# Optimization experiments

Hardware: AMD Instinct MI355X
Metric: run time of the kernel (lower is better)

Reference implementation:

```python
import jax, jax.numpy as jnp
import numpy as np

NUM_EXPERTS = 8
TOP_K = 2
CAPACITY_FACTOR = 1.25


def setup_inputs() -> dict:
    key = jax.random.key(0)
    ks = jax.random.split(key, 5)
    B, S, D, H, E = 4, 2048, 1024, 2048, NUM_EXPERTS
    scale = 0.02
    return {
        "x": jax.random.normal(ks[0], (B, S, D), dtype=jnp.float32),
        "gate_w": jax.random.normal(ks[1], (E, D), dtype=jnp.float32) * scale,
        "gate_proj_w": jax.random.normal(ks[2], (E, H, D), dtype=jnp.float32) * scale,
        "up_proj_w": jax.random.normal(ks[3], (E, H, D), dtype=jnp.float32) * scale,
        "down_proj_w": jax.random.normal(ks[4], (E, D, H), dtype=jnp.float32) * scale,
    }


def reference(x, gate_w, gate_proj_w, up_proj_w, down_proj_w):
    B, S, D = x.shape
    E, K = NUM_EXPERTS, TOP_K
    T = B * S
    xf = x.reshape(T, D)

    # Router: softmax over expert logits, then top-k (eval mode: no aux loss)
    logits = xf @ gate_w.T                      # (T, E)
    probs = jax.nn.softmax(logits, axis=-1)
    top_p, top_i = jax.lax.top_k(probs, K)      # (T, K)
    w = top_p / (jnp.sum(top_p, axis=-1, keepdims=True) + 1e-9)  # (T, K)

    # Capacity drop: per (k, expert), keep only the first `capacity` tokens
    # in token order (matches torch loop which truncates nonzero indices).
    capacity = int(CAPACITY_FACTOR * T / E)
    oh = jax.nn.one_hot(top_i, E, dtype=jnp.int32)        # (T, K, E)
    rank = jnp.cumsum(oh, axis=0) - 1                     # rank within (k, e)
    my_rank = jnp.sum(rank * oh, axis=-1)                 # (T, K)
    keep = (my_rank < capacity).astype(w.dtype)

    # Combined per-token per-expert weight (dropped tokens get 0)
    comb = jnp.einsum("tk,tke->te", w * keep, oh.astype(w.dtype))  # (T, E)

    # Per-expert dense SwiGLU; zero-weight tokens contribute nothing,
    # which matches the masked gather/scatter-add of the original.
    out = jnp.zeros_like(xf)
    for e in range(E):
        g = jax.nn.silu(xf @ gate_proj_w[e].T)   # (T, H)
        u = xf @ up_proj_w[e].T                  # (T, H)
        y = (g * u) @ down_proj_w[e].T           # (T, D)
        out = out + comb[:, e:e + 1] * y
    return out.reshape(B, S, D)
```

## Files before the change

### kernel.cpp

```cpp
#include <hip/hip_runtime.h>
#include <hip/hip_bf16.h>
#include <stdint.h>

#define T_TOK 8192
#define D_DIM 1024
#define H_DIM 2048
#define E_NUM 8
#define CAP   1280
#define CAP2  2560
#define MT_K  10

#define BM 128
#define BN 128
#define BN_GU 64
#define BK 32

typedef __attribute__((ext_vector_type(8))) short short8;
typedef __attribute__((ext_vector_type(4))) float float4v;
typedef __attribute__((address_space(1))) const unsigned int gu32;
typedef __attribute__((address_space(3))) unsigned int lu32;

static __device__ __forceinline__ unsigned short f2bf(float f) {
    unsigned int u = __float_as_uint(f);
    unsigned int r = (u + 0x7FFFu + ((u >> 16) & 1u)) >> 16;
    return (unsigned short)r;
}

static __device__ __forceinline__ void store4bf(unsigned short* d, float4 v) {
    union { unsigned short u[4]; uint2 q; } pk;
    pk.u[0] = f2bf(v.x); pk.u[1] = f2bf(v.y);
    pk.u[2] = f2bf(v.z); pk.u[3] = f2bf(v.w);
    *(uint2*)d = pk.q;
}

__global__ __launch_bounds__(256) void convert_w_k(
    const float* __restrict__ wg, const float* __restrict__ wu,
    const float* __restrict__ wd,
    unsigned short* __restrict__ wgbf, unsigned short* __restrict__ wubf,
    unsigned short* __restrict__ wdbf) {
    const int W4 = E_NUM * H_DIM * D_DIM / 4;
    const int total = 3 * W4;
    const int stride = gridDim.x * 256;
    for (int i = blockIdx.x * 256 + threadIdx.x; i < total; i += stride) {
        const float* s; unsigned short* d; int j;
        if (i < W4)          { s = wg; d = wgbf; j = i; }
        else if (i < 2 * W4) { s = wu; d = wubf; j = i - W4; }
        else                 { s = wd; d = wdbf; j = i - 2 * W4; }
        store4bf(d + (size_t)j * 4, ((const float4*)s)[j]);
    }
}

__global__ __launch_bounds__(256) void router_k(
    const float* __restrict__ x, const float* __restrict__ gw,
    int* __restrict__ topi, float* __restrict__ topw,
    unsigned short* __restrict__ xbf) {
    const int t = blockIdx.x * 4 + (threadIdx.x >> 6);
    const int lane = threadIdx.x & 63;
    const float* xr = x + (size_t)t * D_DIM;
    unsigned short* xbr = xbf + (size_t)t * D_DIM;

    float p[E_NUM];
#pragma unroll
    for (int e = 0; e < E_NUM; ++e) p[e] = 0.f;
#pragma unroll
    for (int c = 0; c < 4; ++c) {
        const int idx = c * 256 + lane * 4;
        const float4 xv = *(const float4*)(xr + idx);
        store4bf(xbr + idx, xv);
#pragma unroll
        for (int e = 0; e < E_NUM; ++e) {
            const float4 gv = *(const float4*)(gw + e * D_DIM + idx);
            p[e] += xv.x * gv.x + xv.y * gv.y + xv.z * gv.z + xv.w * gv.w;
        }
    }
#pragma unroll
    for (int e = 0; e < E_NUM; ++e) {
        float v = p[e];
#pragma unroll
        for (int off = 32; off >= 1; off >>= 1) v += __shfl_xor(v, off);
        p[e] = v;
    }
    if (lane == 0) {
        float mx = p[0];
#pragma unroll
        for (int e = 1; e < E_NUM; ++e) mx = fmaxf(mx, p[e]);
        float pe[E_NUM]; float s = 0.f;
#pragma unroll
        for (int e = 0; e < E_NUM; ++e) { pe[e] = expf(p[e] - mx); s += pe[e]; }
        const float inv = 1.f / s;
        int i0 = 0;
#pragma unroll
        for (int e = 1; e < E_NUM; ++e) if (pe[e] > pe[i0]) i0 = e;
        int i1 = -1;
#pragma unroll
        for (int e = 0; e < E_NUM; ++e) {
            if (e == i0) continue;
            if (i1 < 0 || pe[e] > pe[i1]) i1 = e;
        }
        const float p0 = pe[i0] * inv, p1 = pe[i1] * inv;
        const float wn = 1.f / (p0 + p1 + 1e-9f);
        topi[t * 2 + 0] = i0; topi[t * 2 + 1] = i1;
        topw[t * 2 + 0] = p0 * wn; topw[t * 2 + 1] = p1 * wn;
    }
}

__global__ __launch_bounds__(1024) void assign_k(
    const int* __restrict__ topi, const float* __restrict__ topw,
    int* __restrict__ tok_list, float* __restrict__ w_list,
    int* __restrict__ cnt) {
    __shared__ unsigned char topiL[T_TOK * 2];
    __shared__ int kept[2][E_NUM];
    const int tid = threadIdx.x;
    const int wid = tid >> 6, lane = tid & 63;
    const int k = wid >> 3, e = wid & 7;
    const uint64_t lt = (1ull << lane) - 1ull;

    for (int i = tid; i < T_TOK * 2 / 4; i += 1024) {
        const int4 v = ((const int4*)topi)[i];
        uchar4 b;
        b.x = (unsigned char)v.x; b.y = (unsigned char)v.y;
        b.z = (unsigned char)v.z; b.w = (unsigned char)v.w;
        ((uchar4*)topiL)[i] = b;
    }
    __syncthreads();

    int total = 0;
    for (int base = 0; base < T_TOK; base += 64) {
        const int idx = topiL[(base + lane) * 2 + k];
        total += __popcll(__ballot(idx == e));
    }
    if (lane == 0) {
        const int kc = min(total, CAP);
        kept[k][e] = kc;
        cnt[e * 2 + k] = kc;
    }
    __syncthreads();
    const int myBase = e * CAP2 + k * CAP;

    int running = 0, keptRun = 0;
    for (int base = 0; base < T_TOK; base += 64) {
        const int t = base + lane;
        const bool pred = (topiL[t * 2 + k] == e);
        const uint64_t m = __ballot(pred);
        const int rank = running + __popcll(m & lt);
        const bool keep = pred && (rank < CAP);
        const uint64_t km = __ballot(keep);
        if (keep) {
            const int slot = myBase + keptRun + __popcll(km & lt);
            tok_list[slot] = t;
            w_list[slot] = topw[t * 2 + k];
        }
        running += __popcll(m);
        keptRun += __popcll(km);
    }
    __syncthreads();
    for (int s = tid; s < E_NUM * CAP2; s += 1024) {
        const int ee = s / CAP2;
        const int rem = s - ee * CAP2;
        const int kk = rem / CAP, ls = rem - kk * CAP;
        if (ls >= kept[kk][ee]) { tok_list[s] = 0; w_list[s] = 0.f; }
    }
}

__global__ __launch_bounds__(256, 4) void gateup_bf_k(
    const unsigned short* __restrict__ xbf,
    const unsigned short* __restrict__ wgbf, const unsigned short* __restrict__ wubf,
    const int* __restrict__ tok_list, const int* __restrict__ cnt,
    unsigned short* __restrict__ h_ws, int e0) {
    const int ez = blockIdx.z;
    const int e = e0 + ez;
    const int kk = blockIdx.y / MT_K;
    const int m0 = (blockIdx.y - kk * MT_K) * BM;
    if (m0 >= cnt[e * 2 + kk]) return;
    const int n0 = blockIdx.x * BN_GU;
    const int sbase = e * CAP2 + kk * CAP + m0;
    const size_t hbase = (size_t)ez * CAP2 + kk * CAP + m0;

    __shared__ __align__(1024) unsigned short smem[16384];

    const int tid = threadIdx.x, wid = tid >> 6, lane = tid & 63;

    const unsigned short* gsrc[8];
    int ldsoff[8];
#pragma unroll
    for (int i = 0; i < 8; ++i) {
        const int f = (wid * 8 + i) * 64 + lane;
        const unsigned short* g;
        if (f < 1024) {
            const int r = f >> 3, c = (f & 7) ^ (r & 7);
            const int tok = tok_list[sbase + r];
            g = xbf + (size_t)tok * D_DIM + c * 8;
        } else if (f < 1536) {
            const int fr = f - 1024;
            const int r = fr >> 3, c = (fr & 7) ^ (r & 7);
            g = wgbf + ((size_t)e * H_DIM + n0 + r) * D_DIM + c * 8;
        } else {
            const int fr = f - 1536;
            const int r = fr >> 3, c = (fr & 7) ^ (r & 7);
            g = wubf + ((size_t)e * H_DIM + n0 + r) * D_DIM + c * 8;
        }
        gsrc[i] = g;
        ldsoff[i] = (wid * 8 + i) * 1024;
    }

    float4v accg[4][2], accu[4][2];
#pragma unroll
    for (int i = 0; i < 4; ++i)
#pragma unroll
        for (int j = 0; j < 2; ++j) {
            accg[i][j] = (float4v){0.f, 0.f, 0.f, 0.f};
            accu[i][j] = (float4v){0.f, 0.f, 0.f, 0.f};
        }

    const int wm = (wid & 1) * 64;
    const int wn = (wid >> 1) * 32;
    const int frow = lane & 15;
    const int quad = lane >> 4;

    for (int k0 = 0; k0 < D_DIM; k0 += 64) {
#pragma unroll
        for (int i = 0; i < 8; ++i)
            __builtin_amdgcn_global_load_lds(
                (gu32*)(gsrc[i] + k0),
                (lu32*)((char*)smem + ldsoff[i]), 16, 0, 0);
        __syncthreads();

#pragma unroll
        for (int s = 0; s < 2; ++s) {
            const int c = s * 4 + quad;
            short8 af[4], bgf[2], buf[2];
#pragma unroll
            for (int i = 0; i < 4; ++i) {
                const int row = wm + i * 16 + frow;
                af[i] = *(const short8*)&smem[(row * 8 + (c ^ (row & 7))) * 8];
            }
#pragma unroll
            for (int j = 0; j < 2; ++j) {
                const int row = wn + j * 16 + frow;
                bgf[j] = *(const short8*)&smem[8192 + (row * 8 + (c ^ (row & 7))) * 8];
                buf[j] = *(const short8*)&smem[12288 + (row * 8 + (c ^ (row & 7))) * 8];
            }
#pragma unroll
            for (int i = 0; i < 4; ++i)
#pragma unroll
                for (int j = 0; j < 2; ++j) {
                    accg[i][j] = __builtin_amdgcn_mfma_f32_16x16x32_bf16(af[i], bgf[j], accg[i][j], 0, 0, 0);
                    accu[i][j] = __builtin_amdgcn_mfma_f32_16x16x32_bf16(af[i], buf[j], accu[i][j], 0, 0, 0);
                }
        }
        __syncthreads();
    }

    const int col = lane & 15, rbase = (lane >> 4) * 4;
#pragma unroll
    for (int i = 0; i < 4; ++i)
#pragma unroll
        for (int j = 0; j < 2; ++j)
#pragma unroll
            for (int r = 0; r < 4; ++r) {
                const float g = accg[i][j][r];
                const float u = accu[i][j][r];
                const float hv = (g / (1.f + __expf(-g))) * u;
                const int m = wm + i * 16 + rbase + r;
                const int n = wn + j * 16 + col;
                h_ws[(hbase + m) * H_DIM + (n0 + n)] = f2bf(hv);
            }
}

__global__ __launch_bounds__(256, 3) void down_bf_k(
    const unsigned short* __restrict__ h_ws, const unsigned short* __restrict__ wdbf,
    const int* __restrict__ tok_list, const float* __restrict__ w_list,
    const int* __restrict__ cnt, float* __restrict__ out, int e0, int kk) {
    const int ez = blockIdx.z;
    const int e = e0 + ez;
    const int m0 = blockIdx.y * BM;
    const int nkept = cnt[e * 2 + kk];
    if (m0 >= nkept) return;
    const int n0 = blockIdx.x * BN;
    const int sbase = e * CAP2 + kk * CAP + m0;
    const size_t hbase = (size_t)ez * CAP2 + kk * CAP + m0;

    __shared__ __align__(1024) unsigned short smem[16384];
    __shared__ int tokL[BM];
    __shared__ float wL[BM];

    const int tid = threadIdx.x, wid = tid >> 6, lane = tid & 63;
    if (tid < BM) {
        tokL[tid] = tok_list[sbase + tid];
        wL[tid] = w_list[sbase + tid];
    }

    const unsigned short* gsrc[8];
    int ldsoff[8];
#pragma unroll
    for (int i = 0; i < 8; ++i) {
        const int f = (wid * 8 + i) * 64 + lane;
        const unsigned short* g;
        if (f < 1024) {
            const int r = f >> 3, c = (f & 7) ^ (r & 7);
            g = h_ws + (hbase + r) * H_DIM + c * 8;
        } else {
            const int fr = f - 1024;
            const int r = fr >> 3, c = (fr & 7) ^ (r & 7);
            g = wdbf + ((size_t)e * D_DIM + n0 + r) * H_DIM + c * 8;
        }
        gsrc[i] = g;
        ldsoff[i] = (wid * 8 + i) * 1024;
    }

    float4v acc[4][4];
#pragma unroll
    for (int i = 0; i < 4; ++i)
#pragma unroll
        for (int j = 0; j < 4; ++j) acc[i][j] = (float4v){0.f, 0.f, 0.f, 0.f};

    const int wm = (wid & 1) * 64, wn = (wid >> 1) * 64;
    const int frow = lane & 15;
    const int quad = lane >> 4;

    for (int k0 = 0; k0 < H_DIM; k0 += 64) {
#pragma unroll
        for (int i = 0; i < 8; ++i)
            __builtin_amdgcn_global_load_lds(
                (gu32*)(gsrc[i] + k0),
                (lu32*)((char*)smem + ldsoff[i]), 16, 0, 0);
        __syncthreads();

#pragma unroll
        for (int s = 0; s < 2; ++s) {
            const int c = s * 4 + quad;
            short8 af[4], bf[4];
#pragma unroll
            for (int i = 0; i < 4; ++i) {
                const int row = wm + i * 16 + frow;
                af[i] = *(const short8*)&smem[(row * 8 + (c ^ (row & 7))) * 8];
            }
#pragma unroll
            for (int j = 0; j < 4; ++j) {
                const int row = wn + j * 16 + frow;
                bf[j] = *(const short8*)&smem[8192 + (row * 8 + (c ^ (row & 7))) * 8];
            }
#pragma unroll
            for (int i = 0; i < 4; ++i)
#pragma unroll
                for (int j = 0; j < 4; ++j)
                    acc[i][j] = __builtin_amdgcn_mfma_f32_16x16x32_bf16(af[i], bf[j], acc[i][j], 0, 0, 0);
        }
        __syncthreads();
    }

    const int col = lane & 15, rbase = (lane >> 4) * 4;
#pragma unroll
    for (int i = 0; i < 4; ++i)
#pragma unroll
        for (int r = 0; r < 4; ++r) {
            const int m = wm + i * 16 + rbase + r;
            if (m0 + m >= nkept) continue;
            const float wRow = wL[m];
            float* orow = out + (size_t)tokL[m] * D_DIM + n0;
#pragma unroll
            for (int j = 0; j < 4; ++j) {
                const int n = j * 16 + wn + col;
                const float v = acc[i][j][r] * wRow;
                if (kk == 0) orow[n] = v;
                else         orow[n] += v;
            }
        }
}

__global__ __launch_bounds__(256, 2) void gateup_legacy_k(
    const float* __restrict__ x,
    const float* __restrict__ wg_all, const float* __restrict__ wu_all,
    const int* __restrict__ tok_list, const int* __restrict__ cnt,
    unsigned short* __restrict__ h_ws, int e0) {
    const int ez = blockIdx.z;
    const int e = e0 + ez;
    const int kk = blockIdx.y / MT_K;
    const int m0 = (blockIdx.y - kk * MT_K) * BM;
    if (m0 >= cnt[e * 2 + kk]) return;
    const int n0 = blockIdx.x * BN;
    const int sbase = e * CAP2 + kk * CAP + m0;
    const size_t hbase = (size_t)ez * CAP2 + kk * CAP + m0;

    __shared__ __align__(16) unsigned short As[BM][BK];
    __shared__ __align__(16) unsigned short Bg[BN][BK];
    __shared__ __align__(16) unsigned short Bu[BN][BK];
    __shared__ int tokL[BM];

    const int tid = threadIdx.x;
    if (tid < BM) tokL[tid] = tok_list[sbase + tid];
    __syncthreads();

    const float* wg = wg_all + (size_t)e * H_DIM * D_DIM;
    const float* wu = wu_all + (size_t)e * H_DIM * D_DIM;

    const float* aSrc[4]; const float* gSrc[4]; const float* uSrc[4];
    unsigned short* aDst[4]; unsigned short* gDst[4]; unsigned short* uDst[4];
#pragma unroll
    for (int it = 0; it < 4; ++it) {
        const int fid = it * 256 + tid;
        const int row = fid >> 3;
        const int c4 = (fid & 7) * 4;
        aSrc[it] = x + (size_t)tokL[row] * D_DIM + c4;
        gSrc[it] = wg + (size_t)(n0 + row) * D_DIM + c4;
        uSrc[it] = wu + (size_t)(n0 + row) * D_DIM + c4;
        aDst[it] = &As[row][c4];
        gDst[it] = &Bg[row][c4];
        uDst[it] = &Bu[row][c4];
    }

    float4v accg[4][4], accu[4][4];
#pragma unroll
    for (int i = 0; i < 4; ++i)
#pragma unroll
        for (int j = 0; j < 4; ++j) {
            accg[i][j] = (float4v){0.f, 0.f, 0.f, 0.f};
            accu[i][j] = (float4v){0.f, 0.f, 0.f, 0.f};
        }

    const int wid = tid >> 6, lane = tid & 63;
    const int wm = (wid & 1) * 64, wn = (wid >> 1) * 64;
    const int frow = lane & 15;
    const int fk = (lane >> 4) * 8;

    for (int k0 = 0; k0 < D_DIM; k0 += BK) {
#pragma unroll
        for (int it = 0; it < 4; ++it) {
            store4bf(aDst[it], *(const float4*)(aSrc[it] + k0));
            store4bf(gDst[it], *(const float4*)(gSrc[it] + k0));
            store4bf(uDst[it], *(const float4*)(uSrc[it] + k0));
        }
        __syncthreads();
        short8 af[4], bgf[4], buf[4];
#pragma unroll
        for (int i = 0; i < 4; ++i)
            af[i] = *(const short8*)&As[wm + i * 16 + frow][fk];
#pragma unroll
        for (int j = 0; j < 4; ++j) {
            bgf[j] = *(const short8*)&Bg[wn + j * 16 + frow][fk];
            buf[j] = *(const short8*)&Bu[wn + j * 16 + frow][fk];
        }
#pragma unroll
        for (int i = 0; i < 4; ++i)
#pragma unroll
            for (int j = 0; j < 4; ++j) {
                accg[i][j] = __builtin_amdgcn_mfma_f32_16x16x32_bf16(af[i], bgf[j], accg[i][j], 0, 0, 0);
                accu[i][j] = __builtin_amdgcn_mfma_f32_16x16x32_bf16(af[i], buf[j], accu[i][j], 0, 0, 0);
            }
        __syncthreads();
    }

    const int col = lane & 15, rbase = (lane >> 4) * 4;
#pragma unroll
    for (int i = 0; i < 4; ++i)
#pragma unroll
        for (int j = 0; j < 4; ++j)
#pragma unroll
            for (int r = 0; r < 4; ++r) {
                const float g = accg[i][j][r];
                const float u = accu[i][j][r];
                const float hv = (g / (1.f + __expf(-g))) * u;
                const int m = wm + i * 16 + rbase + r;
                const int n = wn + j * 16 + col;
                h_ws[(hbase + m) * H_DIM + (n0 + n)] = f2bf(hv);
            }
}

__global__ __launch_bounds__(256, 2) void down_legacy_k(
    const unsigned short* __restrict__ h_ws, const float* __restrict__ wd_all,
    const int* __restrict__ tok_list, const float* __restrict__ w_list,
    const int* __restrict__ cnt, float* __restrict__ out, int e0) {
    const int ez = blockIdx.z;
    const int e = e0 + ez;
    const int kk = blockIdx.y / MT_K;
    const int m0 = (blockIdx.y - kk * MT_K) * BM;
    if (m0 >= cnt[e * 2 + kk]) return;
    const int n0 = blockIdx.x * BN;
    const int sbase = e * CAP2 + kk * CAP + m0;
    const size_t hbase = (size_t)ez * CAP2 + kk * CAP + m0;

    __shared__ __align__(16) unsigned short As[BM][BK];
    __shared__ __align__(16) unsigned short Bs[BN][BK];
    __shared__ int tokL[BM];
    __shared__ float wL[BM];

    const int tid = threadIdx.x;
    if (tid < BM) {
        tokL[tid] = tok_list[sbase + tid];
        wL[tid] = w_list[sbase + tid];
    }
    __syncthreads();

    const unsigned short* hA = h_ws + hbase * H_DIM;
    const float* wd = wd_all + (size_t)e * D_DIM * H_DIM;

    const unsigned short* aSrc[2]; unsigned short* aDst[2];
#pragma unroll
    for (int it = 0; it < 2; ++it) {
        const int fid = it * 256 + tid;
        const int row = fid >> 2;
        const int c8 = (fid & 3) * 8;
        aSrc[it] = hA + (size_t)row * H_DIM + c8;
        aDst[it] = &As[row][c8];
    }
    const float* bSrc[4]; unsigned short* bDst[4];
#pragma unroll
    for (int it = 0; it < 4; ++it) {
        const int fid = it * 256 + tid;
        const int row = fid >> 3;
        const int c4 = (fid & 7) * 4;
        bSrc[it] = wd + (size_t)(n0 + row) * H_DIM + c4;
        bDst[it] = &Bs[row][c4];
    }

    float4v acc[4][4];
#pragma unroll
    for (int i = 0; i < 4; ++i)
#pragma unroll
        for (int j = 0; j < 4; ++j) acc[i][j] = (float4v){0.f, 0.f, 0.f, 0.f};

    const int wid = tid >> 6, lane = tid & 63;
    const int wm = (wid & 1) * 64, wn = (wid >> 1) * 64;
    const int frow = lane & 15;
    const int fk = (lane >> 4) * 8;

    for (int k0 = 0; k0 < H_DIM; k0 += BK) {
#pragma unroll
        for (int it = 0; it < 2; ++it)
            *(uint4*)aDst[it] = *(const uint4*)(aSrc[it] + k0);
#pragma unroll
        for (int it = 0; it < 4; ++it)
            store4bf(bDst[it], *(const float4*)(bSrc[it] + k0));
        __syncthreads();
        short8 af[4], bf[4];
#pragma unroll
        for (int i = 0; i < 4; ++i)
            af[i] = *(const short8*)&As[wm + i * 16 + frow][fk];
#pragma unroll
        for (int j = 0; j < 4; ++j)
            bf[j] = *(const short8*)&Bs[wn + j * 16 + frow][fk];
#pragma unroll
        for (int i = 0; i < 4; ++i)
#pragma unroll
            for (int j = 0; j < 4; ++j)
                acc[i][j] = __builtin_amdgcn_mfma_f32_16x16x32_bf16(af[i], bf[j], acc[i][j], 0, 0, 0);
        __syncthreads();
    }

    const int col = lane & 15, rbase = (lane >> 4) * 4;
#pragma unroll
    for (int i = 0; i < 4; ++i)
#pragma unroll
        for (int j = 0; j < 4; ++j)
#pragma unroll
            for (int r = 0; r < 4; ++r) {
                const int m = wm + i * 16 + rbase + r;
                const int n = wn + j * 16 + col;
                const float v = acc[i][j][r] * wL[m];
                unsafeAtomicAdd(&out[(size_t)tokL[m] * D_DIM + n0 + n], v);
            }
}

extern "C" void kernel_launch(void* const* d_in, const int* in_sizes, int n_in,
                              void* d_out, int out_size, void* d_ws, size_t ws_size,
                              hipStream_t stream) {
    const float* x        = (const float*)d_in[0];
    const float* gate_w   = (const float*)d_in[1];
    const float* gate_pw  = (const float*)d_in[2];
    const float* up_pw    = (const float*)d_in[3];
    const float* down_pw  = (const float*)d_in[4];
    float* out = (float*)d_out;
    (void)n_in; (void)in_sizes; (void)out_size;

    uint8_t* ws = (uint8_t*)d_ws;
    size_t off = 0;
    int*   topi     = (int*)(ws + off);   off += (size_t)T_TOK * 2 * 4;
    float* topw     = (float*)(ws + off); off += (size_t)T_TOK * 2 * 4;
    int*   tok_list = (int*)(ws + off);   off += (size_t)E_NUM * CAP2 * 4;
    float* w_list   = (float*)(ws + off); off += (size_t)E_NUM * CAP2 * 4;
    int*   cnt      = (int*)(ws + off);   off += 256;
    off = (off + 4095) & ~(size_t)4095;
    const size_t routing_end = off;

    const size_t x_elems = (size_t)T_TOK * D_DIM;
    const size_t w_elems = (size_t)E_NUM * H_DIM * D_DIM;
    unsigned short* xbf  = (unsigned short*)(ws + off); off += x_elems * 2;
    unsigned short* wgbf = (unsigned short*)(ws + off); off += w_elems * 2;
    unsigned short* wubf = (unsigned short*)(ws + off); off += w_elems * 2;
    unsigned short* wdbf = (unsigned short*)(ws + off); off += w_elems * 2;
    const size_t need_base = off;
    const size_t per_e = (size_t)CAP2 * H_DIM * 2;

    hipMemsetAsync(out, 0, (size_t)T_TOK * D_DIM * sizeof(float), stream);

    if (ws_size >= need_base + per_e) {
        unsigned short* h_ws = (unsigned short*)(ws + need_base);
        int chunk = (int)((ws_size - need_base) / per_e);
        if (chunk > E_NUM) chunk = E_NUM;

        router_k<<<T_TOK / 4, 256, 0, stream>>>(x, gate_w, topi, topw, xbf);
        assign_k<<<1, 1024, 0, stream>>>(topi, topw, tok_list, w_list, cnt);
        convert_w_k<<<4096, 256, 0, stream>>>(gate_pw, up_pw, down_pw,
                                              wgbf, wubf, wdbf);

        for (int e0 = 0; e0 < E_NUM; e0 += chunk) {
            const int ne = (e0 + chunk <= E_NUM) ? chunk : (E_NUM - e0);
            dim3 g1(H_DIM / BN_GU, 2 * MT_K, ne);
            gateup_bf_k<<<g1, 256, 0, stream>>>(xbf, wgbf, wubf, tok_list, cnt, h_ws, e0);
            dim3 g2(D_DIM / BN, MT_K, ne);
            down_bf_k<<<g2, 256, 0, stream>>>(h_ws, wdbf, tok_list, w_list, cnt, out, e0, 0);
            down_bf_k<<<g2, 256, 0, stream>>>(h_ws, wdbf, tok_list, w_list, cnt, out, e0, 1);
        }
    } else {
        unsigned short* h_ws = (unsigned short*)(ws + routing_end);
        int chunk = (ws_size > routing_end) ? (int)((ws_size - routing_end) / per_e) : 0;
        if (chunk > E_NUM) chunk = E_NUM;
        if (chunk < 1) chunk = 1;

        router_k<<<T_TOK / 4, 256, 0, stream>>>(x, gate_w, topi, topw, xbf);
        assign_k<<<1, 1024, 0, stream>>>(topi, topw, tok_list, w_list, cnt);

        for (int e0 = 0; e0 < E_NUM; e0 += chunk) {
            const int ne = (e0 + chunk <= E_NUM) ? chunk : (E_NUM - e0);
            dim3 g1(H_DIM / BN, 2 * MT_K, ne);
            gateup_legacy_k<<<g1, 256, 0, stream>>>(x, gate_pw, up_pw, tok_list, cnt, h_ws, e0);
            dim3 g2(D_DIM / BN, 2 * MT_K, ne);
            down_legacy_k<<<g2, 256, 0, stream>>>(h_ws, down_pw, tok_list, w_list, cnt, out, e0);
        }
    }
}
```

Before: 604.8 us.

## Fuse router with weight conversion and merge down-proj launches via atomics

Merges the router and the fp32-to-bf16 weight conversion into one prep kernel so routing blocks and conversion blocks run in the same grid. Stages the SwiGLU output tile through shared memory so h_ws gets 16-byte coalesced stores. Collapses the two per-k down-projection launches into one grid with k in blockIdx.z, using atomic adds into the pre-zeroed output, and raises the occupancy hint to 4. The atomics add contention and make the float summation order nondeterministic. The prep kernel also now writes its outputs into buffers that the routing-assignment kernel reads.

```diff
diff --git a/kernel.cpp b/kernel.cpp
--- a/kernel.cpp
+++ b/kernel.cpp
@@ -15,6 +15,9 @@
 #define BN_GU 64
 #define BK 32
 
+#define ROUTE_BLKS (T_TOK / 4)
+#define CONV_BLKS  4096
+
 typedef __attribute__((ext_vector_type(8))) short short8;
 typedef __attribute__((ext_vector_type(4))) float float4v;
 typedef __attribute__((address_space(1))) const unsigned int gu32;
@@ -33,20 +36,75 @@
     *(uint2*)d = pk.q;
 }
 
-__global__ __launch_bounds__(256) void convert_w_k(
+__global__ __launch_bounds__(256) void prep_k(
+    const float* __restrict__ x, const float* __restrict__ gw,
+    int* __restrict__ topi, float* __restrict__ topw,
+    unsigned short* __restrict__ xbf,
     const float* __restrict__ wg, const float* __restrict__ wu,
     const float* __restrict__ wd,
     unsigned short* __restrict__ wgbf, unsigned short* __restrict__ wubf,
     unsigned short* __restrict__ wdbf) {
-    const int W4 = E_NUM * H_DIM * D_DIM / 4;
-    const int total = 3 * W4;
-    const int stride = gridDim.x * 256;
-    for (int i = blockIdx.x * 256 + threadIdx.x; i < total; i += stride) {
-        const float* s; unsigned short* d; int j;
-        if (i < W4)          { s = wg; d = wgbf; j = i; }
-        else if (i < 2 * W4) { s = wu; d = wubf; j = i - W4; }
-        else                 { s = wd; d = wdbf; j = i - 2 * W4; }
-        store4bf(d + (size_t)j * 4, ((const float4*)s)[j]);
+    if (blockIdx.x < ROUTE_BLKS) {
+        const int t = blockIdx.x * 4 + (threadIdx.x >> 6);
+        const int lane = threadIdx.x & 63;
+        const float* xr = x + (size_t)t * D_DIM;
+        unsigned short* xbr = xbf + (size_t)t * D_DIM;
+
+        float p[E_NUM];
+#pragma unroll
+        for (int e = 0; e < E_NUM; ++e) p[e] = 0.f;
+#pragma unroll
+        for (int c = 0; c < 4; ++c) {
+            const int idx = c * 256 + lane * 4;
+            const float4 xv = *(const float4*)(xr + idx);
+            store4bf(xbr + idx, xv);
+#pragma unroll
+            for (int e = 0; e < E_NUM; ++e) {
+                const float4 gv = *(const float4*)(gw + e * D_DIM + idx);
+                p[e] += xv.x * gv.x + xv.y * gv.y + xv.z * gv.z + xv.w * gv.w;
+            }
+        }
+#pragma unroll
+        for (int e = 0; e < E_NUM; ++e) {
+            float v = p[e];
+#pragma unroll
+            for (int off = 32; off >= 1; off >>= 1) v += __shfl_xor(v, off);
+            p[e] = v;
+        }
+        if (lane == 0) {
+            float mx = p[0];
+#pragma unroll
+            for (int e = 1; e < E_NUM; ++e) mx = fmaxf(mx, p[e]);
+            float pe[E_NUM]; float s = 0.f;
+#pragma unroll
+            for (int e = 0; e < E_NUM; ++e) { pe[e] = expf(p[e] - mx); s += pe[e]; }
+            const float inv = 1.f / s;
+            int i0 = 0;
+#pragma unroll
+            for (int e = 1; e < E_NUM; ++e) if (pe[e] > pe[i0]) i0 = e;
+            int i1 = -1;
+#pragma unroll
+            for (int e = 0; e < E_NUM; ++e) {
+                if (e == i0) continue;
+                if (i1 < 0 || pe[e] > pe[i1]) i1 = e;
+            }
+            const float p0 = pe[i0] * inv, p1 = pe[i1] * inv;
+            const float wn = 1.f / (p0 + p1 + 1e-9f);
+            topi[t * 2 + 0] = i0; topi[t * 2 + 1] = i1;
+            topw[t * 2 + 0] = p0 * wn; topw[t * 2 + 1] = p1 * wn;
+        }
+    } else {
+        const int W4 = E_NUM * H_DIM * D_DIM / 4;
+        const int total = 3 * W4;
+        const int stride = CONV_BLKS * 256;
+        for (int i = (blockIdx.x - ROUTE_BLKS) * 256 + threadIdx.x; i < total;
+             i += stride) {
+            const float* s; unsigned short* d; int j;
+            if (i < W4)          { s = wg; d = wgbf; j = i; }
+            else if (i < 2 * W4) { s = wu; d = wubf; j = i - W4; }
+            else                 { s = wd; d = wdbf; j = i - 2 * W4; }
+            store4bf(d + (size_t)j * 4, ((const float4*)s)[j]);
+        }
     }
 }
 
@@ -263,15 +321,24 @@
                 const float hv = (g / (1.f + __expf(-g))) * u;
                 const int m = wm + i * 16 + rbase + r;
                 const int n = wn + j * 16 + col;
-                h_ws[(hbase + m) * H_DIM + (n0 + n)] = f2bf(hv);
-            }
-}
-
-__global__ __launch_bounds__(256, 3) void down_bf_k(
+                smem[m * 64 + n] = f2bf(hv);
+            }
+    __syncthreads();
+#pragma unroll
+    for (int c2 = 0; c2 < 4; ++c2) {
+        const int idx = c2 * 256 + tid;
+        const int row = idx >> 3, cc = (idx & 7) * 8;
+        *(uint4*)&h_ws[(hbase + row) * H_DIM + n0 + cc] =
+            *(const uint4*)&smem[row * 64 + cc];
+    }
+}
+
+__global__ __launch_bounds__(256, 4) void down_bf_k(
     const unsigned short* __restrict__ h_ws, const unsigned short* __restrict__ wdbf,
     const int* __restrict__ tok_list, const float* __restrict__ w_list,
-    const int* __restrict__ cnt, float* __restrict__ out, int e0, int kk) {
-    const int ez = blockIdx.z;
+    const int* __restrict__ cnt, float* __restrict__ out, int e0) {
+    const int ez = blockIdx.z >> 1;
+    const int kk = blockIdx.z & 1;
     const int e = e0 + ez;
     const int m0 = blockIdx.y * BM;
     const int nkept = cnt[e * 2 + kk];
@@ -361,9 +428,7 @@
 #pragma unroll
             for (int j = 0; j < 4; ++j) {
                 const int n = j * 16 + wn + col;
-                const float v = acc[i][j][r] * wRow;
-                if (kk == 0) orow[n] = v;
-                else         orow[n] += v;
+                unsafeAtomicAdd(&orow[n], acc[i][j][r] * wRow);
             }
         }
 }
@@ -598,18 +663,17 @@
         int chunk = (int)((ws_size - need_base) / per_e);
         if (chunk > E_NUM) chunk = E_NUM;
 
-        router_k<<<T_TOK / 4, 256, 0, stream>>>(x, gate_w, topi, topw, xbf);
+        prep_k<<<ROUTE_BLKS + CONV_BLKS, 256, 0, stream>>>(
+            x, gate_w, topi, topw, xbf,
+            gate_pw, up_pw, down_pw, wgbf, wubf, wdbf);
         assign_k<<<1, 1024, 0, stream>>>(topi, topw, tok_list, w_list, cnt);
-        convert_w_k<<<4096, 256, 0, stream>>>(gate_pw, up_pw, down_pw,
-                                              wgbf, wubf, wdbf);
 
         for (int e0 = 0; e0 < E_NUM; e0 += chunk) {
             const int ne = (e0 + chunk <= E_NUM) ? chunk : (E_NUM - e0);
             dim3 g1(H_DIM / BN_GU, 2 * MT_K, ne);
             gateup_bf_k<<<g1, 256, 0, stream>>>(xbf, wgbf, wubf, tok_list, cnt, h_ws, e0);
-            dim3 g2(D_DIM / BN, MT_K, ne);
-            down_bf_k<<<g2, 256, 0, stream>>>(h_ws, wdbf, tok_list, w_list, cnt, out, e0, 0);
-            down_bf_k<<<g2, 256, 0, stream>>>(h_ws, wdbf, tok_list, w_list, cnt, out, e0, 1);
+            dim3 g2(D_DIM / BN, MT_K, 2 * ne);
+            down_bf_k<<<g2, 256, 0, stream>>>(h_ws, wdbf, tok_list, w_list, cnt, out, e0);
         }
     } else {
         unsigned short* h_ws = (unsigned short*)(ws + routing_end);
```

New measurement: 878.6 us. 45.3% more time.
